# Optimization experiments

Measured on AMD Instinct MI355X. Metric: run time of the kernel, lower is better.

Reference implementation:

```python
import jax, jax.numpy as jnp
import numpy as np
from jax import lax

T, H, I, E = 1024, 2048, 1024, 16
G, TOPK_GROUP, TOP_K = 4, 2, 4
ROUTED_SCALE = 2.5
W_SCALE = 0.02  # keep activations in a sane range


def setup_inputs() -> dict:
    key = jax.random.key(0)
    ks = jax.random.split(key, 7)
    return {
        "hidden_states": jax.random.normal(ks[0], (T, H), jnp.float32),
        "gate_w": jax.random.normal(ks[1], (E, H), jnp.float32) * W_SCALE,
        "e_bias": jax.random.normal(ks[2], (E,), jnp.float32),
        "w_gate_up": jax.random.normal(ks[3], (E, 2 * I, H), jnp.float32) * W_SCALE,
        "w_down": jax.random.normal(ks[4], (E, H, I), jnp.float32) * W_SCALE,
        "shared_w_gate_up": jax.random.normal(ks[5], (2 * I, H), jnp.float32) * W_SCALE,
        "shared_w_down": jax.random.normal(ks[6], (H, I), jnp.float32) * W_SCALE,
    }


def _grouped_topk(scores, e_bias):
    # scores: sigmoid router scores [T, E]
    scores_b = scores + e_bias[None, :]
    # group score = sum of top-2 biased scores within each group (bias branch)
    group_scores = jnp.sum(lax.top_k(scores_b.reshape(-1, G, E // G), 2)[0], axis=-1)  # [T, G]
    _, group_idx = lax.top_k(group_scores, TOPK_GROUP)  # [T, topk_group]
    group_mask = jnp.any(jax.nn.one_hot(group_idx, G, dtype=jnp.bool_), axis=1)  # [T, G]
    score_mask = jnp.repeat(group_mask, E // G, axis=-1)  # [T, E]
    tmp = jnp.where(score_mask, scores_b, 0.0)
    _, topk_ids = lax.top_k(tmp, TOP_K)  # [T, K]
    topk_w = jnp.take_along_axis(scores, topk_ids, axis=1)  # weights from UNbiased scores
    topk_w = topk_w / jnp.sum(topk_w, axis=-1, keepdims=True)  # renormalize
    return topk_w, topk_ids


def _silu_and_mul(gu):
    g, u = jnp.split(gu, 2, axis=-1)
    return jax.nn.silu(g) * u


def reference(hidden_states, gate_w, e_bias, w_gate_up, w_down,
              shared_w_gate_up, shared_w_down):
    x = hidden_states  # [T, H]
    # shared expert MLP
    shared = _silu_and_mul(x @ shared_w_gate_up.T) @ shared_w_down.T  # [T, H]
    # router
    logits = x @ gate_w.T                      # [T, E]
    scores = jax.nn.sigmoid(logits)
    topk_w, topk_ids = _grouped_topk(scores, e_bias)
    # dense combine weights [T, E] (zero for unselected experts)
    combine = jnp.zeros((T, E), x.dtype).at[jnp.arange(T)[:, None], topk_ids].add(topk_w)
    # routed experts: SwiGLU per expert, combined with routing weights
    gu = jnp.einsum('th,eih->tei', x, w_gate_up)        # [T, E, 2I]
    a = _silu_and_mul(gu)                               # [T, E, I]
    routed = jnp.einsum('tei,ehi,te->th', a, w_down, combine)  # [T, H]
    return routed * ROUTED_SCALE + shared
```

## Files before the change

### kernel.cpp

```cpp
#include <hip/hip_runtime.h>
#include <math.h>

typedef __bf16 bf16;
typedef bf16 bf16x4 __attribute__((ext_vector_type(4)));
typedef bf16 bf16x8 __attribute__((ext_vector_type(8)));
typedef float f32x4 __attribute__((ext_vector_type(4)));

#define T_TOK   1024
#define H_DIM   2048
#define I_DIM   1024
#define E_NUM   16
#define NPAIR_R 4096
#define NPAIR   5120
#define LDSS    40

__global__ __launch_bounds__(256) void router_kernel(
    const float* __restrict__ x, const float* __restrict__ gate_w,
    const float* __restrict__ e_bias,
    int* __restrict__ topk_ids, float* __restrict__ topk_w,
    int* __restrict__ counts)
{
  int t = blockIdx.x;
  int tid = threadIdx.x;
  float acc[16];
#pragma unroll
  for (int e = 0; e < 16; ++e) acc[e] = 0.f;
  const float* xr = x + (size_t)t * H_DIM;
  for (int h = tid; h < H_DIM; h += 256) {
    float xv = xr[h];
#pragma unroll
    for (int e = 0; e < 16; ++e) acc[e] += xv * gate_w[e * H_DIM + h];
  }
#pragma unroll
  for (int e = 0; e < 16; ++e) {
#pragma unroll
    for (int off = 32; off >= 1; off >>= 1)
      acc[e] += __shfl_down(acc[e], off, 64);
  }
  __shared__ float red[4][16];
  int lane = tid & 63, wave = tid >> 6;
  if (lane == 0) {
#pragma unroll
    for (int e = 0; e < 16; ++e) red[wave][e] = acc[e];
  }
  __syncthreads();
  if (tid == 0) {
    float scores[16], sb[16];
    for (int e = 0; e < 16; ++e) {
      float l = red[0][e] + red[1][e] + red[2][e] + red[3][e];
      float s = 1.f / (1.f + expf(-l));
      scores[e] = s;
      sb[e] = s + e_bias[e];
    }
    float gs[4];
    for (int g = 0; g < 4; ++g) {
      float b1 = -1e30f, b2 = -1e30f;
      for (int j = 0; j < 4; ++j) {
        float v = sb[g * 4 + j];
        if (v > b1) { b2 = b1; b1 = v; }
        else if (v > b2) b2 = v;
      }
      gs[g] = b1 + b2;
    }
    int g1 = 0; float bv = gs[0];
    for (int g = 1; g < 4; ++g) if (gs[g] > bv) { bv = gs[g]; g1 = g; }
    int g2 = -1; float bv2 = -1e30f;
    for (int g = 0; g < 4; ++g) if (g != g1 && gs[g] > bv2) { bv2 = gs[g]; g2 = g; }
    float tmp[16];
    for (int e = 0; e < 16; ++e) {
      int grp = e >> 2;
      tmp[e] = (grp == g1 || grp == g2) ? sb[e] : 0.0f;
    }
    bool used[16] = {false};
    int ids[4]; float wv[4]; float wsum = 0.f;
    for (int k = 0; k < 4; ++k) {
      int bi = 0; float bvv = -1e30f;
      for (int i = 0; i < 16; ++i)
        if (!used[i] && tmp[i] > bvv) { bvv = tmp[i]; bi = i; }
      used[bi] = true;
      ids[k] = bi; wv[k] = scores[bi]; wsum += scores[bi];
    }
    float inv = 1.f / wsum;
    for (int k = 0; k < 4; ++k) {
      topk_ids[t * 4 + k] = ids[k];
      topk_w[t * 4 + k] = wv[k] * inv;
      atomicAdd(&counts[ids[k]], 1);
    }
  }
}

__global__ void offsets_kernel(const int* __restrict__ counts, int* __restrict__ off)
{
  if (threadIdx.x == 0 && blockIdx.x == 0) {
    int s = 0;
    for (int e = 0; e < 16; ++e) { off[e] = s; s += counts[e]; }
    off[16] = s;
  }
}

__global__ __launch_bounds__(256) void scatter_kernel(
    const int* __restrict__ topk_ids, const float* __restrict__ topk_w,
    const int* __restrict__ off, int* __restrict__ cursor,
    int* __restrict__ pair_token, float* __restrict__ pair_scale)
{
  int i = blockIdx.x * 256 + threadIdx.x;
  if (i < NPAIR_R) {
    int e = topk_ids[i];
    float w = topk_w[i];
    int pos = atomicAdd(&cursor[e], 1);
    int idx = off[e] + pos;
    pair_token[idx] = i >> 2;
    pair_scale[idx] = 2.5f * w;
  } else if (i < NPAIR) {
    pair_token[i] = i - NPAIR_R;
    pair_scale[i] = 1.0f;
  }
}

__global__ __launch_bounds__(256) void gateup_kernel(
    const float* __restrict__ x, const float* __restrict__ w_gu,
    const float* __restrict__ s_wgu,
    const int* __restrict__ off, const int* __restrict__ pair_token,
    bf16* __restrict__ gu_buf)
{
  const int nt = blockIdx.x;
  const int mt = blockIdx.y;
  const int e  = blockIdx.z;
  const int poff = (e < 16) ? off[e]     : NPAIR_R;
  const int pend = (e < 16) ? off[e + 1] : NPAIR;
  const int cnt  = pend - poff;
  if (mt * 128 >= cnt) return;
  const float* __restrict__ B = (e < 16) ? (w_gu + (size_t)e * 2 * I_DIM * H_DIM) : s_wgu;

  __shared__ bf16 As[128 * LDSS];
  __shared__ bf16 Bs[128 * LDSS];

  const int tid = threadIdx.x;
  const int lane = tid & 63, wave = tid >> 6;
  const int wm = wave >> 1, wn = wave & 1;
  const int srow = tid >> 1;
  const int scol = (tid & 1) * 16;

  int rloc = mt * 128 + srow;
  int p_eff = poff + (rloc < cnt ? rloc : cnt - 1);
  const float* __restrict__ Arow = x + (size_t)pair_token[p_eff] * H_DIM;
  const float* __restrict__ Brow = B + (size_t)(nt * 128 + srow) * H_DIM;

  f32x4 acc[4][4];
  f32x4 zz = {0.f, 0.f, 0.f, 0.f};
#pragma unroll
  for (int mi = 0; mi < 4; ++mi)
#pragma unroll
    for (int ni = 0; ni < 4; ++ni) acc[mi][ni] = zz;

  for (int k0 = 0; k0 < H_DIM; k0 += 32) {
#pragma unroll
    for (int i = 0; i < 4; ++i) {
      float4 av = *(const float4*)(Arow + k0 + scol + 4 * i);
      float4 bv = *(const float4*)(Brow + k0 + scol + 4 * i);
      bf16x4 a4, b4;
      a4[0] = (bf16)av.x; a4[1] = (bf16)av.y; a4[2] = (bf16)av.z; a4[3] = (bf16)av.w;
      b4[0] = (bf16)bv.x; b4[1] = (bf16)bv.y; b4[2] = (bf16)bv.z; b4[3] = (bf16)bv.w;
      *(bf16x4*)(&As[srow * LDSS + scol + 4 * i]) = a4;
      *(bf16x4*)(&Bs[srow * LDSS + scol + 4 * i]) = b4;
    }
    __syncthreads();
    const int kq = (lane >> 4) * 8;
    bf16x8 af[4], bfv[4];
#pragma unroll
    for (int mi = 0; mi < 4; ++mi)
      af[mi] = *(const bf16x8*)(&As[(wm * 64 + mi * 16 + (lane & 15)) * LDSS + kq]);
#pragma unroll
    for (int ni = 0; ni < 4; ++ni)
      bfv[ni] = *(const bf16x8*)(&Bs[(wn * 64 + ni * 16 + (lane & 15)) * LDSS + kq]);
#pragma unroll
    for (int mi = 0; mi < 4; ++mi)
#pragma unroll
      for (int ni = 0; ni < 4; ++ni)
        acc[mi][ni] = __builtin_amdgcn_mfma_f32_16x16x32_bf16(af[mi], bfv[ni], acc[mi][ni], 0, 0, 0);
    __syncthreads();
  }

  const int colb = nt * 128 + wn * 64;
#pragma unroll
  for (int mi = 0; mi < 4; ++mi) {
#pragma unroll
    for (int reg = 0; reg < 4; ++reg) {
      int r = wm * 64 + mi * 16 + ((lane >> 4) * 4) + reg;
      int rl = mt * 128 + r;
      if (rl < cnt) {
        size_t p = (size_t)(poff + rl);
        bf16* orow = gu_buf + p * (2 * I_DIM) + colb + (lane & 15);
#pragma unroll
        for (int ni = 0; ni < 4; ++ni)
          orow[ni * 16] = (bf16)acc[mi][ni][reg];
      }
    }
  }
}

__global__ __launch_bounds__(256) void silu_kernel(
    const bf16* __restrict__ gu, bf16* __restrict__ a)
{
  int idx = (blockIdx.x * 256 + threadIdx.x) * 4;
  int p = idx >> 10;
  int c = idx & 1023;
  const bf16* g = gu + (size_t)p * (2 * I_DIM) + c;
  bf16x4 g4 = *(const bf16x4*)(g);
  bf16x4 u4 = *(const bf16x4*)(g + I_DIM);
  bf16x4 r;
#pragma unroll
  for (int j = 0; j < 4; ++j) {
    float gf = (float)g4[j];
    float uf = (float)u4[j];
    float s = gf / (1.f + expf(-gf));
    r[j] = (bf16)(s * uf);
  }
  *(bf16x4*)(a + idx) = r;
}

__global__ __launch_bounds__(256) void down_kernel(
    const bf16* __restrict__ a_buf, const float* __restrict__ w_dn,
    const float* __restrict__ s_wdn,
    const int* __restrict__ off, const int* __restrict__ pair_token,
    const float* __restrict__ pair_scale, float* __restrict__ out)
{
  const int nt = blockIdx.x;
  const int mt = blockIdx.y;
  const int e  = blockIdx.z;
  const int poff = (e < 16) ? off[e]     : NPAIR_R;
  const int pend = (e < 16) ? off[e + 1] : NPAIR;
  const int cnt  = pend - poff;
  if (mt * 128 >= cnt) return;
  const float* __restrict__ B = (e < 16) ? (w_dn + (size_t)e * H_DIM * I_DIM) : s_wdn;

  __shared__ bf16 As[128 * LDSS];
  __shared__ bf16 Bs[128 * LDSS];

  const int tid = threadIdx.x;
  const int lane = tid & 63, wave = tid >> 6;
  const int wm = wave >> 1, wn = wave & 1;
  const int srow = tid >> 1;
  const int scol = (tid & 1) * 16;

  const bf16* __restrict__ Arow = a_buf + (size_t)(poff + mt * 128 + srow) * I_DIM;
  const float* __restrict__ Brow = B + (size_t)(nt * 128 + srow) * I_DIM;

  f32x4 acc[4][4];
  f32x4 zz = {0.f, 0.f, 0.f, 0.f};
#pragma unroll
  for (int mi = 0; mi < 4; ++mi)
#pragma unroll
    for (int ni = 0; ni < 4; ++ni) acc[mi][ni] = zz;

  for (int k0 = 0; k0 < I_DIM; k0 += 32) {
    bf16x8 a0 = *(const bf16x8*)(Arow + k0 + scol);
    bf16x8 a1 = *(const bf16x8*)(Arow + k0 + scol + 8);
    *(bf16x8*)(&As[srow * LDSS + scol])     = a0;
    *(bf16x8*)(&As[srow * LDSS + scol + 8]) = a1;
#pragma unroll
    for (int i = 0; i < 4; ++i) {
      float4 bv = *(const float4*)(Brow + k0 + scol + 4 * i);
      bf16x4 b4;
      b4[0] = (bf16)bv.x; b4[1] = (bf16)bv.y; b4[2] = (bf16)bv.z; b4[3] = (bf16)bv.w;
      *(bf16x4*)(&Bs[srow * LDSS + scol + 4 * i]) = b4;
    }
    __syncthreads();
    const int kq = (lane >> 4) * 8;
    bf16x8 af[4], bfv[4];
#pragma unroll
    for (int mi = 0; mi < 4; ++mi)
      af[mi] = *(const bf16x8*)(&As[(wm * 64 + mi * 16 + (lane & 15)) * LDSS + kq]);
#pragma unroll
    for (int ni = 0; ni < 4; ++ni)
      bfv[ni] = *(const bf16x8*)(&Bs[(wn * 64 + ni * 16 + (lane & 15)) * LDSS + kq]);
#pragma unroll
    for (int mi = 0; mi < 4; ++mi)
#pragma unroll
      for (int ni = 0; ni < 4; ++ni)
        acc[mi][ni] = __builtin_amdgcn_mfma_f32_16x16x32_bf16(af[mi], bfv[ni], acc[mi][ni], 0, 0, 0);
    __syncthreads();
  }

  const int colb = nt * 128 + wn * 64;
#pragma unroll
  for (int mi = 0; mi < 4; ++mi) {
#pragma unroll
    for (int reg = 0; reg < 4; ++reg) {
      int r = wm * 64 + mi * 16 + ((lane >> 4) * 4) + reg;
      int rl = mt * 128 + r;
      if (rl < cnt) {
        int p = poff + rl;
        int tok = pair_token[p];
        float sc = pair_scale[p];
        float* orow = out + (size_t)tok * H_DIM + colb + (lane & 15);
#pragma unroll
        for (int ni = 0; ni < 4; ++ni)
          atomicAdd(&orow[ni * 16], acc[mi][ni][reg] * sc);
      }
    }
  }
}

extern "C" void kernel_launch(void* const* d_in, const int* in_sizes, int n_in,
                              void* d_out, int out_size, void* d_ws, size_t ws_size,
                              hipStream_t stream)
{
  const float* x     = (const float*)d_in[0];
  const float* gatew = (const float*)d_in[1];
  const float* ebias = (const float*)d_in[2];
  const float* w_gu  = (const float*)d_in[3];
  const float* w_dn  = (const float*)d_in[4];
  const float* s_wgu = (const float*)d_in[5];
  const float* s_wdn = (const float*)d_in[6];
  float* out = (float*)d_out;

  char* ws = (char*)d_ws;
  int*   off        = (int*)(ws + 0);
  int*   counts     = (int*)(ws + 128);
  int*   cursor     = (int*)(ws + 192);
  int*   topk_ids   = (int*)(ws + 256);
  float* topk_w     = (float*)(ws + 16640);
  int*   pair_token = (int*)(ws + 33024);
  float* pair_scale = (float*)(ws + 53504);
  bf16*  gu_buf     = (bf16*)(ws + 73984);
  bf16*  a_buf      = (bf16*)(ws + 73984 + 20971520);

  hipMemsetAsync(out, 0, (size_t)T_TOK * H_DIM * sizeof(float), stream);
  hipMemsetAsync(ws + 128, 0, 128, stream);

  router_kernel<<<T_TOK, 256, 0, stream>>>(x, gatew, ebias, topk_ids, topk_w, counts);
  offsets_kernel<<<1, 64, 0, stream>>>(counts, off);
  scatter_kernel<<<NPAIR / 256, 256, 0, stream>>>(topk_ids, topk_w, off, cursor,
                                                  pair_token, pair_scale);
  dim3 g1(16, 8, 17);
  gateup_kernel<<<g1, 256, 0, stream>>>(x, w_gu, s_wgu, off, pair_token, gu_buf);
  silu_kernel<<<(NPAIR * I_DIM) / (256 * 4), 256, 0, stream>>>(gu_buf, a_buf);
  dim3 g2(16, 8, 17);
  down_kernel<<<g2, 256, 0, stream>>>(a_buf, w_dn, s_wdn, off, pair_token, pair_scale, out);
}
```

Baseline: 661.8 us.

## Double-buffer GEMM tiles via global_load_lds and fuse SiLU into gate-up epilogue

Both expert GEMMs now stage A and B tiles into LDS with direct global-to-LDS 16-byte loads. They use double buffering and an XOR swizzle, so the next tile's loads overlap the current tile's MFMA work. The router also writes a bf16 copy of x for the gate-up kernel to load, replacing per-tile fp32 conversion. Gate and up columns are interleaved within each block, so the SiLU-and-multiply happens in the epilogue and the separate silu kernel and the full gate-up buffer are removed. The trade-offs are larger LDS use (fp32 B tiles, double-buffered) with fp32-to-bf16 conversion moved to the LDS read path, and gathered A rows past the segment end are no longer clamped.

After: 646.2 us. 2.4% less time.

```diff
diff --git a/kernel.cpp b/kernel.cpp
--- a/kernel.cpp
+++ b/kernel.cpp
@@ -12,11 +12,16 @@
 #define E_NUM   16
 #define NPAIR_R 4096
 #define NPAIR   5120
-#define LDSS    40
+
+typedef __attribute__((address_space(3))) unsigned int lds_uint;
+typedef __attribute__((address_space(1))) const unsigned int gbl_uint;
+__device__ __forceinline__ void gld16(const void* g, void* l) {
+  __builtin_amdgcn_global_load_lds((gbl_uint*)g, (lds_uint*)l, 16, 0, 0);
+}
 
 __global__ __launch_bounds__(256) void router_kernel(
     const float* __restrict__ x, const float* __restrict__ gate_w,
-    const float* __restrict__ e_bias,
+    const float* __restrict__ e_bias, bf16* __restrict__ xb,
     int* __restrict__ topk_ids, float* __restrict__ topk_w,
     int* __restrict__ counts)
 {
@@ -26,8 +31,10 @@
 #pragma unroll
   for (int e = 0; e < 16; ++e) acc[e] = 0.f;
   const float* xr = x + (size_t)t * H_DIM;
+  bf16* xbr = xb + (size_t)t * H_DIM;
   for (int h = tid; h < H_DIM; h += 256) {
     float xv = xr[h];
+    xbr[h] = (bf16)xv;
 #pragma unroll
     for (int e = 0; e < 16; ++e) acc[e] += xv * gate_w[e * H_DIM + h];
   }
@@ -117,11 +124,11 @@
   }
 }
 
-__global__ __launch_bounds__(256) void gateup_kernel(
-    const float* __restrict__ x, const float* __restrict__ w_gu,
+__global__ __launch_bounds__(256, 3) void gateup_kernel(
+    const bf16* __restrict__ xb, const float* __restrict__ w_gu,
     const float* __restrict__ s_wgu,
     const int* __restrict__ off, const int* __restrict__ pair_token,
-    bf16* __restrict__ gu_buf)
+    bf16* __restrict__ a_buf)
 {
   const int nt = blockIdx.x;
   const int mt = blockIdx.y;
@@ -132,19 +139,46 @@
   if (mt * 128 >= cnt) return;
   const float* __restrict__ B = (e < 16) ? (w_gu + (size_t)e * 2 * I_DIM * H_DIM) : s_wgu;
 
-  __shared__ bf16 As[128 * LDSS];
-  __shared__ bf16 Bs[128 * LDSS];
+  __shared__ __align__(16) bf16  As[2][128 * 32];
+  __shared__ __align__(16) float Bs[2][128 * 32];
 
   const int tid = threadIdx.x;
-  const int lane = tid & 63, wave = tid >> 6;
+  const int lane = tid & 63;
+  const int wave = tid >> 6;
   const int wm = wave >> 1, wn = wave & 1;
-  const int srow = tid >> 1;
-  const int scol = (tid & 1) * 16;
-
-  int rloc = mt * 128 + srow;
-  int p_eff = poff + (rloc < cnt ? rloc : cnt - 1);
-  const float* __restrict__ Arow = x + (size_t)pair_token[p_eff] * H_DIM;
-  const float* __restrict__ Brow = B + (size_t)(nt * 128 + srow) * H_DIM;
+  const int c0 = lane >> 4;
+  const int fr = lane & 15;
+
+  const bf16* aptr[2];
+#pragma unroll
+  for (int s = 0; s < 2; ++s) {
+    int idx = s * 256 + tid;
+    int ar = idx >> 2, ach = idx & 3;
+    int sch = ach ^ ((ar >> 1) & 3);
+    int p = poff + mt * 128 + ar;
+    aptr[s] = xb + (size_t)pair_token[p] * H_DIM + sch * 8;
+  }
+  const float* bptr[4];
+#pragma unroll
+  for (int s = 0; s < 4; ++s) {
+    int idx = s * 256 + tid;
+    int br = idx >> 3, bch = idx & 7;
+    int sch = bch ^ (br & 7);
+    int rg = nt * 64 + br + (br >= 64 ? 960 : 0);
+    bptr[s] = B + (size_t)rg * H_DIM + sch * 4;
+  }
+  int a_off[4];
+#pragma unroll
+  for (int mi = 0; mi < 4; ++mi) {
+    int ar = wm * 64 + mi * 16 + fr;
+    a_off[mi] = ar * 64 + ((c0 ^ ((ar >> 1) & 3)) << 4);
+  }
+  int b_off[4];
+#pragma unroll
+  for (int ni = 0; ni < 4; ++ni) {
+    int br = wn * 32 + (ni & 1) * 16 + fr + (ni >> 1) * 64;
+    b_off[ni] = br * 128 + (((2 * c0) ^ (br & 7)) << 4);
+  }
 
   f32x4 acc[4][4];
   f32x4 zz = {0.f, 0.f, 0.f, 0.f};
@@ -153,73 +187,73 @@
 #pragma unroll
     for (int ni = 0; ni < 4; ++ni) acc[mi][ni] = zz;
 
-  for (int k0 = 0; k0 < H_DIM; k0 += 32) {
-#pragma unroll
-    for (int i = 0; i < 4; ++i) {
-      float4 av = *(const float4*)(Arow + k0 + scol + 4 * i);
-      float4 bv = *(const float4*)(Brow + k0 + scol + 4 * i);
-      bf16x4 a4, b4;
-      a4[0] = (bf16)av.x; a4[1] = (bf16)av.y; a4[2] = (bf16)av.z; a4[3] = (bf16)av.w;
-      b4[0] = (bf16)bv.x; b4[1] = (bf16)bv.y; b4[2] = (bf16)bv.z; b4[3] = (bf16)bv.w;
-      *(bf16x4*)(&As[srow * LDSS + scol + 4 * i]) = a4;
-      *(bf16x4*)(&Bs[srow * LDSS + scol + 4 * i]) = b4;
-    }
+  const int ldso = tid * 16;
+#pragma unroll
+  for (int s = 0; s < 2; ++s)
+    gld16(aptr[s], (char*)(&As[0][0]) + s * 4096 + ldso);
+#pragma unroll
+  for (int s = 0; s < 4; ++s)
+    gld16(bptr[s], (char*)(&Bs[0][0]) + s * 4096 + ldso);
+  __syncthreads();
+
+  int cur = 0;
+  const int NT = H_DIM / 32;
+  for (int t = 0; t < NT; ++t) {
+    if (t + 1 < NT) {
+      const int k0 = (t + 1) * 32;
+#pragma unroll
+      for (int s = 0; s < 2; ++s)
+        gld16(aptr[s] + k0, (char*)(&As[cur ^ 1][0]) + s * 4096 + ldso);
+#pragma unroll
+      for (int s = 0; s < 4; ++s)
+        gld16(bptr[s] + k0, (char*)(&Bs[cur ^ 1][0]) + s * 4096 + ldso);
+    }
+    const char* Ab = (const char*)(&As[cur][0]);
+    const char* Bb = (const char*)(&Bs[cur][0]);
+    bf16x8 af[4], bv[4];
+#pragma unroll
+    for (int mi = 0; mi < 4; ++mi)
+      af[mi] = *(const bf16x8*)(Ab + a_off[mi]);
+#pragma unroll
+    for (int ni = 0; ni < 4; ++ni) {
+      f32x4 x0 = *(const f32x4*)(Bb + b_off[ni]);
+      f32x4 x1 = *(const f32x4*)(Bb + (b_off[ni] ^ 16));
+      bf16x8 b;
+      b[0] = (bf16)x0[0]; b[1] = (bf16)x0[1]; b[2] = (bf16)x0[2]; b[3] = (bf16)x0[3];
+      b[4] = (bf16)x1[0]; b[5] = (bf16)x1[1]; b[6] = (bf16)x1[2]; b[7] = (bf16)x1[3];
+      bv[ni] = b;
+    }
+#pragma unroll
+    for (int mi = 0; mi < 4; ++mi)
+#pragma unroll
+      for (int ni = 0; ni < 4; ++ni)
+        acc[mi][ni] = __builtin_amdgcn_mfma_f32_16x16x32_bf16(af[mi], bv[ni], acc[mi][ni], 0, 0, 0);
     __syncthreads();
-    const int kq = (lane >> 4) * 8;
-    bf16x8 af[4], bfv[4];
-#pragma unroll
-    for (int mi = 0; mi < 4; ++mi)
-      af[mi] = *(const bf16x8*)(&As[(wm * 64 + mi * 16 + (lane & 15)) * LDSS + kq]);
-#pragma unroll
-    for (int ni = 0; ni < 4; ++ni)
-      bfv[ni] = *(const bf16x8*)(&Bs[(wn * 64 + ni * 16 + (lane & 15)) * LDSS + kq]);
-#pragma unroll
-    for (int mi = 0; mi < 4; ++mi)
-#pragma unroll
-      for (int ni = 0; ni < 4; ++ni)
-        acc[mi][ni] = __builtin_amdgcn_mfma_f32_16x16x32_bf16(af[mi], bfv[ni], acc[mi][ni], 0, 0, 0);
-    __syncthreads();
-  }
-
-  const int colb = nt * 128 + wn * 64;
+    cur ^= 1;
+  }
+
 #pragma unroll
   for (int mi = 0; mi < 4; ++mi) {
 #pragma unroll
     for (int reg = 0; reg < 4; ++reg) {
-      int r = wm * 64 + mi * 16 + ((lane >> 4) * 4) + reg;
+      int r = wm * 64 + mi * 16 + c0 * 4 + reg;
       int rl = mt * 128 + r;
       if (rl < cnt) {
         size_t p = (size_t)(poff + rl);
-        bf16* orow = gu_buf + p * (2 * I_DIM) + colb + (lane & 15);
-#pragma unroll
-        for (int ni = 0; ni < 4; ++ni)
-          orow[ni * 16] = (bf16)acc[mi][ni][reg];
+        bf16* orow = a_buf + p * I_DIM + nt * 64 + wn * 32 + fr;
+#pragma unroll
+        for (int ni = 0; ni < 2; ++ni) {
+          float g = acc[mi][ni][reg];
+          float u = acc[mi][ni + 2][reg];
+          float sg = g / (1.f + expf(-g));
+          orow[ni * 16] = (bf16)(sg * u);
+        }
       }
     }
   }
 }
 
-__global__ __launch_bounds__(256) void silu_kernel(
-    const bf16* __restrict__ gu, bf16* __restrict__ a)
-{
-  int idx = (blockIdx.x * 256 + threadIdx.x) * 4;
-  int p = idx >> 10;
-  int c = idx & 1023;
-  const bf16* g = gu + (size_t)p * (2 * I_DIM) + c;
-  bf16x4 g4 = *(const bf16x4*)(g);
-  bf16x4 u4 = *(const bf16x4*)(g + I_DIM);
-  bf16x4 r;
-#pragma unroll
-  for (int j = 0; j < 4; ++j) {
-    float gf = (float)g4[j];
-    float uf = (float)u4[j];
-    float s = gf / (1.f + expf(-gf));
-    r[j] = (bf16)(s * uf);
-  }
-  *(bf16x4*)(a + idx) = r;
-}
-
-__global__ __launch_bounds__(256) void down_kernel(
+__global__ __launch_bounds__(256, 3) void down_kernel(
     const bf16* __restrict__ a_buf, const float* __restrict__ w_dn,
     const float* __restrict__ s_wdn,
     const int* __restrict__ off, const int* __restrict__ pair_token,
@@ -234,17 +268,45 @@
   if (mt * 128 >= cnt) return;
   const float* __restrict__ B = (e < 16) ? (w_dn + (size_t)e * H_DIM * I_DIM) : s_wdn;
 
-  __shared__ bf16 As[128 * LDSS];
-  __shared__ bf16 Bs[128 * LDSS];
+  __shared__ __align__(16) bf16  As[2][128 * 32];
+  __shared__ __align__(16) float Bs[2][128 * 32];
 
   const int tid = threadIdx.x;
-  const int lane = tid & 63, wave = tid >> 6;
+  const int lane = tid & 63;
+  const int wave = tid >> 6;
   const int wm = wave >> 1, wn = wave & 1;
-  const int srow = tid >> 1;
-  const int scol = (tid & 1) * 16;
-
-  const bf16* __restrict__ Arow = a_buf + (size_t)(poff + mt * 128 + srow) * I_DIM;
-  const float* __restrict__ Brow = B + (size_t)(nt * 128 + srow) * I_DIM;
+  const int c0 = lane >> 4;
+  const int fr = lane & 15;
+
+  const bf16* aptr[2];
+#pragma unroll
+  for (int s = 0; s < 2; ++s) {
+    int idx = s * 256 + tid;
+    int ar = idx >> 2, ach = idx & 3;
+    int sch = ach ^ ((ar >> 1) & 3);
+    int p = poff + mt * 128 + ar;
+    aptr[s] = a_buf + (size_t)p * I_DIM + sch * 8;
+  }
+  const float* bptr[4];
+#pragma unroll
+  for (int s = 0; s < 4; ++s) {
+    int idx = s * 256 + tid;
+    int br = idx >> 3, bch = idx & 7;
+    int sch = bch ^ (br & 7);
+    bptr[s] = B + (size_t)(nt * 128 + br) * I_DIM + sch * 4;
+  }
+  int a_off[4];
+#pragma unroll
+  for (int mi = 0; mi < 4; ++mi) {
+    int ar = wm * 64 + mi * 16 + fr;
+    a_off[mi] = ar * 64 + ((c0 ^ ((ar >> 1) & 3)) << 4);
+  }
+  int b_off[4];
+#pragma unroll
+  for (int ni = 0; ni < 4; ++ni) {
+    int br = wn * 64 + ni * 16 + fr;
+    b_off[ni] = br * 128 + (((2 * c0) ^ (br & 7)) << 4);
+  }
 
   f32x4 acc[4][4];
   f32x4 zz = {0.f, 0.f, 0.f, 0.f};
@@ -253,33 +315,49 @@
 #pragma unroll
     for (int ni = 0; ni < 4; ++ni) acc[mi][ni] = zz;
 
-  for (int k0 = 0; k0 < I_DIM; k0 += 32) {
-    bf16x8 a0 = *(const bf16x8*)(Arow + k0 + scol);
-    bf16x8 a1 = *(const bf16x8*)(Arow + k0 + scol + 8);
-    *(bf16x8*)(&As[srow * LDSS + scol])     = a0;
-    *(bf16x8*)(&As[srow * LDSS + scol + 8]) = a1;
-#pragma unroll
-    for (int i = 0; i < 4; ++i) {
-      float4 bv = *(const float4*)(Brow + k0 + scol + 4 * i);
-      bf16x4 b4;
-      b4[0] = (bf16)bv.x; b4[1] = (bf16)bv.y; b4[2] = (bf16)bv.z; b4[3] = (bf16)bv.w;
-      *(bf16x4*)(&Bs[srow * LDSS + scol + 4 * i]) = b4;
-    }
+  const int ldso = tid * 16;
+#pragma unroll
+  for (int s = 0; s < 2; ++s)
+    gld16(aptr[s], (char*)(&As[0][0]) + s * 4096 + ldso);
+#pragma unroll
+  for (int s = 0; s < 4; ++s)
+    gld16(bptr[s], (char*)(&Bs[0][0]) + s * 4096 + ldso);
+  __syncthreads();
+
+  int cur = 0;
+  const int NT = I_DIM / 32;
+  for (int t = 0; t < NT; ++t) {
+    if (t + 1 < NT) {
+      const int k0 = (t + 1) * 32;
+#pragma unroll
+      for (int s = 0; s < 2; ++s)
+        gld16(aptr[s] + k0, (char*)(&As[cur ^ 1][0]) + s * 4096 + ldso);
+#pragma unroll
+      for (int s = 0; s < 4; ++s)
+        gld16(bptr[s] + k0, (char*)(&Bs[cur ^ 1][0]) + s * 4096 + ldso);
+    }
+    const char* Ab = (const char*)(&As[cur][0]);
+    const char* Bb = (const char*)(&Bs[cur][0]);
+    bf16x8 af[4], bv[4];
+#pragma unroll
+    for (int mi = 0; mi < 4; ++mi)
+      af[mi] = *(const bf16x8*)(Ab + a_off[mi]);
+#pragma unroll
+    for (int ni = 0; ni < 4; ++ni) {
+      f32x4 x0 = *(const f32x4*)(Bb + b_off[ni]);
+      f32x4 x1 = *(const f32x4*)(Bb + (b_off[ni] ^ 16));
+      bf16x8 b;
+      b[0] = (bf16)x0[0]; b[1] = (bf16)x0[1]; b[2] = (bf16)x0[2]; b[3] = (bf16)x0[3];
+      b[4] = (bf16)x1[0]; b[5] = (bf16)x1[1]; b[6] = (bf16)x1[2]; b[7] = (bf16)x1[3];
+      bv[ni] = b;
+    }
+#pragma unroll
+    for (int mi = 0; mi < 4; ++mi)
+#pragma unroll
+      for (int ni = 0; ni < 4; ++ni)
+        acc[mi][ni] = __builtin_amdgcn_mfma_f32_16x16x32_bf16(af[mi], bv[ni], acc[mi][ni], 0, 0, 0);
     __syncthreads();
-    const int kq = (lane >> 4) * 8;
-    bf16x8 af[4], bfv[4];
-#pragma unroll
-    for (int mi = 0; mi < 4; ++mi)
-      af[mi] = *(const bf16x8*)(&As[(wm * 64 + mi * 16 + (lane & 15)) * LDSS + kq]);
-#pragma unroll
-    for (int ni = 0; ni < 4; ++ni)
-      bfv[ni] = *(const bf16x8*)(&Bs[(wn * 64 + ni * 16 + (lane & 15)) * LDSS + kq]);
-#pragma unroll
-    for (int mi = 0; mi < 4; ++mi)
-#pragma unroll
-      for (int ni = 0; ni < 4; ++ni)
-        acc[mi][ni] = __builtin_amdgcn_mfma_f32_16x16x32_bf16(af[mi], bfv[ni], acc[mi][ni], 0, 0, 0);
-    __syncthreads();
+    cur ^= 1;
   }
 
   const int colb = nt * 128 + wn * 64;
@@ -287,13 +365,13 @@
   for (int mi = 0; mi < 4; ++mi) {
 #pragma unroll
     for (int reg = 0; reg < 4; ++reg) {
-      int r = wm * 64 + mi * 16 + ((lane >> 4) * 4) + reg;
+      int r = wm * 64 + mi * 16 + c0 * 4 + reg;
       int rl = mt * 128 + r;
       if (rl < cnt) {
         int p = poff + rl;
         int tok = pair_token[p];
         float sc = pair_scale[p];
-        float* orow = out + (size_t)tok * H_DIM + colb + (lane & 15);
+        float* orow = out + (size_t)tok * H_DIM + colb + fr;
 #pragma unroll
         for (int ni = 0; ni < 4; ++ni)
           atomicAdd(&orow[ni * 16], acc[mi][ni][reg] * sc);
@@ -323,19 +401,18 @@
   float* topk_w     = (float*)(ws + 16640);
   int*   pair_token = (int*)(ws + 33024);
   float* pair_scale = (float*)(ws + 53504);
-  bf16*  gu_buf     = (bf16*)(ws + 73984);
-  bf16*  a_buf      = (bf16*)(ws + 73984 + 20971520);
+  bf16*  x_bf16     = (bf16*)(ws + 73984);
+  bf16*  a_buf      = (bf16*)(ws + 73984 + 4194304);
 
   hipMemsetAsync(out, 0, (size_t)T_TOK * H_DIM * sizeof(float), stream);
   hipMemsetAsync(ws + 128, 0, 128, stream);
 
-  router_kernel<<<T_TOK, 256, 0, stream>>>(x, gatew, ebias, topk_ids, topk_w, counts);
+  router_kernel<<<T_TOK, 256, 0, stream>>>(x, gatew, ebias, x_bf16, topk_ids, topk_w, counts);
   offsets_kernel<<<1, 64, 0, stream>>>(counts, off);
   scatter_kernel<<<NPAIR / 256, 256, 0, stream>>>(topk_ids, topk_w, off, cursor,
                                                   pair_token, pair_scale);
   dim3 g1(16, 8, 17);
-  gateup_kernel<<<g1, 256, 0, stream>>>(x, w_gu, s_wgu, off, pair_token, gu_buf);
-  silu_kernel<<<(NPAIR * I_DIM) / (256 * 4), 256, 0, stream>>>(gu_buf, a_buf);
+  gateup_kernel<<<g1, 256, 0, stream>>>(x_bf16, w_gu, s_wgu, off, pair_token, a_buf);
   dim3 g2(16, 8, 17);
   down_kernel<<<g2, 256, 0, stream>>>(a_buf, w_dn, s_wdn, off, pair_token, pair_scale, out);
 }
```
